# Performance work log

Hardware: AMD Instinct MI355X
Metric: run time of the kernel (lower is better)

## Reference

```python
import jax, jax.numpy as jnp
from jax import lax
import numpy as np

# ---- module hyperparameters (from init_kwargs) ----
DIM = 256
DIM_HEAD = 64
HEADS = 4
GROUPS = 4                      # offset_groups (defaults to heads)
INNER = DIM_HEAD * HEADS        # 256
OFF_DIMS = INNER // GROUPS      # 64
DOWN = 4
KS = 6
PAD = (KS - DOWN) // 2          # 1
OFFSET_SCALE = float(DOWN)      # offset_scale defaults to down_sample_factor
CPB_DIM = DIM // 4              # 64
SCALE = DIM_HEAD ** -0.5


def make_grid(h, w, dtype):
    # torch.meshgrid(arange(w), arange(h), indexing='xy') stacked at dim 0:
    # channel 0 = x (column index), channel 1 = y (row index); shape [2,h,w]
    yy, xx = jnp.meshgrid(jnp.arange(h), jnp.arange(w), indexing='ij')
    return jnp.stack([xx, yy], axis=0).astype(dtype)


def normalize_grid_c(vg):
    # vg: [..., 2, h, w] -> [..., h, w, 2]; faithful to source: channel 0
    # normalized by (h-1), channel 1 by (w-1) (source's h/w naming quirk).
    h, w = vg.shape[-2:]
    gh = 2.0 * vg[..., 0, :, :] / max(h - 1, 1) - 1.0
    gw = 2.0 * vg[..., 1, :, :] / max(w - 1, 1) - 1.0
    return jnp.stack([gh, gw], axis=-1)


def grid_sample_zeros(img, grid):
    # F.grid_sample bilinear, padding_mode='zeros', align_corners=False
    # img: [N,C,H,W]; grid: [N,Hg,Wg,2] with (..,0)=x, (..,1)=y in [-1,1]
    N, C, H, W = img.shape
    ix = ((grid[..., 0] + 1.0) * W - 1.0) * 0.5
    iy = ((grid[..., 1] + 1.0) * H - 1.0) * 0.5
    x0 = jnp.floor(ix)
    y0 = jnp.floor(iy)

    def gather(yy, xx):
        valid = (xx >= 0) & (xx <= W - 1) & (yy >= 0) & (yy <= H - 1)
        xc = jnp.clip(xx, 0, W - 1).astype(jnp.int32)
        yc = jnp.clip(yy, 0, H - 1).astype(jnp.int32)
        vals = jax.vmap(lambda im, y_, x_: im[:, y_, x_])(img, yc, xc)  # [N,C,Hg,Wg]
        return vals * valid[:, None, :, :].astype(img.dtype)

    wa = (x0 + 1 - ix) * (y0 + 1 - iy)
    wb = (ix - x0) * (y0 + 1 - iy)
    wc = (x0 + 1 - ix) * (iy - y0)
    wd = (ix - x0) * (iy - y0)
    return (gather(y0, x0) * wa[:, None]
            + gather(y0, x0 + 1) * wb[:, None]
            + gather(y0 + 1, x0) * wc[:, None]
            + gather(y0 + 1, x0 + 1) * wd[:, None])


def gconv1x1(t, w):
    # grouped 1x1 conv (no bias): t [b, G*Ci, h, w], w [G, Co, Ci]
    G, Co, Ci = w.shape
    bb, _, hh, ww = t.shape
    tg = t.reshape(bb, G, Ci, hh, ww)
    return jnp.einsum('bgihw,goi->bgohw', tg, w).reshape(bb, G * Co, hh, ww)


def setup_inputs() -> dict:
    key = jax.random.key(0)
    ks = jax.random.split(key, 12)
    s = 0.02
    B, H, W = 8, 32, 32
    cg = DIM // GROUPS  # per-group in-channels = 64
    og = INNER // GROUPS  # per-group out-channels = 64
    return {
        'x': jax.random.normal(ks[0], (B, DIM, H, W), jnp.float32),
        'wq': jax.random.normal(ks[1], (GROUPS, og, cg), jnp.float32) * s,
        'wk': jax.random.normal(ks[2], (GROUPS, og, cg), jnp.float32) * s,
        'wv': jax.random.normal(ks[3], (GROUPS, og, cg), jnp.float32) * s,
        'w_off_dw': jax.random.normal(ks[4], (OFF_DIMS, 1, KS, KS), jnp.float32) * s,
        'b_off_dw': jnp.zeros((OFF_DIMS,), jnp.float32),
        'w_off_pw': jax.random.normal(ks[5], (2, OFF_DIMS), jnp.float32) * s,
        'cpb_w1': jax.random.normal(ks[6], (CPB_DIM, 2), jnp.float32) * s,
        'cpb_b1': jnp.zeros((CPB_DIM,), jnp.float32),
        'cpb_w2': jax.random.normal(ks[7], (CPB_DIM, CPB_DIM), jnp.float32) * s,
        'cpb_b2': jnp.zeros((CPB_DIM,), jnp.float32),
        'cpb_w3': jax.random.normal(ks[8], (HEADS // GROUPS, CPB_DIM), jnp.float32) * s,
        'cpb_b3': jnp.zeros((HEADS // GROUPS,), jnp.float32),
        'w_out': jax.random.normal(ks[9], (DIM, INNER), jnp.float32) * s,
        'b_out': jnp.zeros((DIM,), jnp.float32),
    }


def reference(x, wq, wk, wv, w_off_dw, b_off_dw, w_off_pw,
              cpb_w1, cpb_b1, cpb_w2, cpb_b2, cpb_w3, cpb_b3,
              w_out, b_out):
    b, _, H, W = x.shape

    q = gconv1x1(x, wq)                                       # [b, INNER, H, W]
    gq = q.reshape(b * GROUPS, OFF_DIMS, H, W)                # grouped queries
    gx = x.reshape(b * GROUPS, DIM // GROUPS, H, W)           # grouped input

    # to_offsets: depthwise conv -> GELU -> 1x1 conv -> tanh -> scale
    off = lax.conv_general_dilated(
        gq, w_off_dw, window_strides=(DOWN, DOWN),
        padding=[(PAD, PAD), (PAD, PAD)],
        dimension_numbers=('NCHW', 'OIHW', 'NCHW'),
        feature_group_count=OFF_DIMS)
    off = off + b_off_dw[None, :, None, None]
    off = jax.nn.gelu(off, approximate=False)
    off = jnp.einsum('bchw,oc->bohw', off, w_off_pw)
    off = jnp.tanh(off) * OFFSET_SCALE                        # [bg, 2, h2, w2]

    h2, w2 = off.shape[-2:]
    vg = make_grid(h2, w2, off.dtype)[None] + off             # [bg, 2, h2, w2]
    vgs = normalize_grid_c(vg)                                # [bg, h2, w2, 2]

    kv = grid_sample_zeros(gx, vgs)                           # [bg, DIM/G, h2, w2]
    kv = kv.reshape(b, DIM, h2, w2)
    k = gconv1x1(kv, wk)
    v = gconv1x1(kv, wv)
    q = q * SCALE

    def to_heads(t):
        bb, _, hh, ww = t.shape
        return t.reshape(bb, HEADS, DIM_HEAD, hh * ww).transpose(0, 1, 3, 2)

    qh, kh, vh = to_heads(q), to_heads(k), to_heads(v)        # [b, h, i|j, d]
    sim = jnp.einsum('bhid,bhjd->bhij', qh, kh)               # [b, h, HW, h2*w2]

    # CPB relative position bias
    grid_q = normalize_grid_c(make_grid(H, W, x.dtype)).reshape(1, H * W, 2)
    grid_kv = vgs.reshape(b * GROUPS, h2 * w2, 2)
    pos = grid_q[:, :, None, :] - grid_kv[:, None, :, :]      # [bg, i, j, 2]
    bias = jnp.sign(pos) * jnp.log1p(jnp.abs(pos))
    bias = jax.nn.relu(bias @ cpb_w1.T + cpb_b1)
    bias = jax.nn.relu(bias @ cpb_w2.T + cpb_b2)
    bias = bias @ cpb_w3.T + cpb_b3                           # [bg, i, j, o]
    o = HEADS // GROUPS
    bias = bias.reshape(b, GROUPS, H * W, h2 * w2, o)
    bias = bias.transpose(0, 1, 4, 2, 3).reshape(b, HEADS, H * W, h2 * w2)

    attn = jax.nn.softmax(sim + bias, axis=-1)
    out = jnp.einsum('bhij,bhjd->bhid', attn, vh)             # [b, h, HW, d]
    out = out.transpose(0, 1, 3, 2).reshape(b, INNER, H, W)
    out = jnp.einsum('bchw,oc->bohw', out, w_out) + b_out[None, :, None, None]
    return out
```

## Files before the change

### kernel.cpp

```cpp
#include <hip/hip_runtime.h>
#include <hip/hip_bf16.h>
#include <math.h>

#define QSCALE 0.125f

typedef __attribute__((ext_vector_type(8))) short short8b;
typedef __attribute__((ext_vector_type(8))) _Float16 half8;
typedef __attribute__((ext_vector_type(2))) _Float16 half2v;
typedef __attribute__((ext_vector_type(4))) float f32x4;

__device__ __forceinline__ uint pack2(float a, float b) {
    uint r;
    asm("v_cvt_pk_bf16_f32 %0, %1, %2" : "=v"(r) : "v"(a), "v"(b));
    return r;
}
__device__ __forceinline__ uint pkrtz(float a, float b) {
    uint r;
    asm("v_cvt_pkrtz_f16_f32 %0, %1, %2" : "=v"(r) : "v"(a), "v"(b));
    return r;
}
__device__ __forceinline__ half2v h2(uint u) { return __builtin_bit_cast(half2v, u); }
__device__ __forceinline__ float slogf_(float p) {
    return copysignf(log1pf(fabsf(p)), p);
}

__global__ __launch_bounds__(256) void k_qproj(const float* __restrict__ x,
                                               const float* __restrict__ wq,
                                               float* __restrict__ q,
                                               short* __restrict__ qbt) {
    __shared__ float Wst[64 * 68];
    __shared__ float xs[64 * 68];
    int ht = blockIdx.x, g = blockIdx.y, b = blockIdx.z;
    int tid = threadIdx.x;
    for (int e = tid; e < 4096; e += 256) {
        int co = e >> 6, ci = e & 63;
        Wst[ci * 68 + co] = wq[(g * 64 + co) * 64 + ci];
    }
    const float* xb = x + (b * 256 + g * 64) * 1024 + ht * 64;
    for (int e = tid; e < 1024; e += 256) {
        int ci = e >> 4, hq = e & 15;
        *(float4*)&xs[ci * 68 + hq * 4] = *(const float4*)&xb[ci * 1024 + hq * 4];
    }
    __syncthreads();
    int cg = tid >> 4, hg = tid & 15;
    int co0 = cg * 4, hw0 = hg * 4;
    float acc[4][4] = {};
    for (int ci = 0; ci < 64; ci++) {
        float4 a4 = *(float4*)&Wst[ci * 68 + co0];
        float4 b4 = *(float4*)&xs[ci * 68 + hw0];
        float av[4] = {a4.x, a4.y, a4.z, a4.w};
        float bv[4] = {b4.x, b4.y, b4.z, b4.w};
        #pragma unroll
        for (int a = 0; a < 4; a++)
            #pragma unroll
            for (int c = 0; c < 4; c++) acc[a][c] += av[a] * bv[c];
    }
    float* qb = q + (b * 256 + g * 64) * 1024 + ht * 64;
    for (int a = 0; a < 4; a++) {
        float4 o = {acc[a][0], acc[a][1], acc[a][2], acc[a][3]};
        *(float4*)&qb[(co0 + a) * 1024 + hw0] = o;
    }
    short* q16 = qbt + ((size_t)((b * 4 + g) * 1024 + ht * 64)) * 64;
    for (int c = 0; c < 4; c++) {
        uint2 uu;
        uu.x = pack2(acc[0][c] * QSCALE, acc[1][c] * QSCALE);
        uu.y = pack2(acc[2][c] * QSCALE, acc[3][c] * QSCALE);
        *(uint2*)&q16[(hw0 + c) * 64 + co0] = uu;
    }
}

__global__ __launch_bounds__(256) void k_dw(const float* __restrict__ q,
                                            const float* __restrict__ wdw,
                                            const float* __restrict__ bdw,
                                            float* __restrict__ gdw) {
    __shared__ float qs[8 * 1024];
    __shared__ float wds[8 * 36];
    int cg = blockIdx.x, n = blockIdx.y;
    int b = n >> 2, gg = n & 3;
    int c0 = cg * 8;
    int tid = threadIdx.x;
    const float* qn = q + (b * 256 + gg * 64 + c0) * 1024;
    for (int e = tid; e < 2048; e += 256)
        ((float4*)qs)[e] = ((const float4*)qn)[e];
    for (int e = tid; e < 288; e += 256)
        wds[e] = wdw[c0 * 36 + e];
    __syncthreads();
    for (int e = tid; e < 512; e += 256) {
        int c = e >> 6, pos = e & 63;
        int oy = pos >> 3, ox = pos & 7;
        float acc = bdw[c0 + c];
        #pragma unroll
        for (int ky = 0; ky < 6; ky++) {
            int iy = oy * 4 - 1 + ky;
            if (iy < 0 || iy > 31) continue;
            #pragma unroll
            for (int kx = 0; kx < 6; kx++) {
                int ix = ox * 4 - 1 + kx;
                if (ix < 0 || ix > 31) continue;
                acc += qs[c * 1024 + iy * 32 + ix] * wds[c * 36 + ky * 6 + kx];
            }
        }
        gdw[(n * 64 + c0 + c) * 64 + pos] = acc * 0.5f * (1.f + erff(acc * 0.70710678118654752f));
    }
}

__global__ __launch_bounds__(256) void k_pre(const float* __restrict__ x,
                                             const float* __restrict__ gdw,
                                             const float* __restrict__ wpw,
                                             const float* __restrict__ wk,
                                             const float* __restrict__ wv,
                                             const float* __restrict__ wout,
                                             const float* __restrict__ w2,
                                             float* __restrict__ vgs,
                                             uint* __restrict__ u0g,
                                             short* __restrict__ kob,
                                             short* __restrict__ vob,
                                             short* __restrict__ wob,
                                             uint* __restrict__ w2h) {
    __shared__ float gstage[4096];
    __shared__ float kvsT[64 * 68];
    __shared__ uint wkh[64 * 36];
    __shared__ uint wvh[64 * 36];
    __shared__ uint kvh[64 * 36];
    __shared__ float vx_s[64], vy_s[64];
    int n = blockIdx.x, tid = threadIdx.x;
    int b = n >> 2, g = n & 3;

    {
        int e = n * 2048 + tid * 8;
        float4 f0 = *(const float4*)&wout[e];
        float4 f1 = *(const float4*)&wout[e + 4];
        uint4 u = {pack2(f0.x, f0.y), pack2(f0.z, f0.w), pack2(f1.x, f1.y), pack2(f1.z, f1.w)};
        *(uint4*)&wob[e] = u;
    }
    if (tid < 128) {
        int idx = n * 128 + tid;
        int c2 = idx >> 5, p = idx & 31;
        float2 wv2 = *(const float2*)&w2[c2 * 64 + 2 * p];
        w2h[c2 * 32 + p] = pkrtz(wv2.x, wv2.y);
    }
    for (int e = tid; e < 2048; e += 256) {
        int co = e >> 5, p = e & 31;
        float2 a = *(const float2*)&wk[(g * 64 + co) * 64 + 2 * p];
        float2 c = *(const float2*)&wv[(g * 64 + co) * 64 + 2 * p];
        wkh[co * 36 + p] = pkrtz(a.x, a.y);
        wvh[co * 36 + p] = pkrtz(c.x, c.y);
    }
    for (int e = tid; e < 1024; e += 256)
        ((float4*)gstage)[e] = ((const float4*)(gdw + n * 4096))[e];
    __syncthreads();
    if (tid < 128) {
        int o = tid >> 6, pos = tid & 63;
        float a = 0.f;
        #pragma unroll 8
        for (int c = 0; c < 64; c++) a += gstage[c * 64 + pos] * wpw[o * 64 + c];
        float off = tanhf(a) * 4.0f;
        if (o == 0) {
            int ox = pos & 7;
            float v = 2.f * ((float)ox + off) / 7.f - 1.f;
            vx_s[pos] = v;
            vgs[(n * 64 + pos) * 2] = v;
        } else {
            int oy = pos >> 3;
            float v = 2.f * ((float)oy + off) / 7.f - 1.f;
            vy_s[pos] = v;
            vgs[(n * 64 + pos) * 2 + 1] = v;
        }
    }
    __syncthreads();
    for (int e = tid; e < 2048; e += 256) {
        int ix = e >> 6, j = e & 63;
        float qx = (2.f / 31.f) * (float)ix - 1.f;
        float u = slogf_(qx - vx_s[j]);
        u0g[n * 2048 + e] = pkrtz(u, u);
    }
    for (int e = tid; e < 4096; e += 256) {
        int c = e >> 6, pos = e & 63;
        float ix = (vx_s[pos] + 1.f) * 16.f - 0.5f;
        float iy = (vy_s[pos] + 1.f) * 16.f - 0.5f;
        float x0 = floorf(ix), y0 = floorf(iy);
        float wa = (x0 + 1.f - ix) * (y0 + 1.f - iy);
        float wb = (ix - x0) * (y0 + 1.f - iy);
        float wc = (x0 + 1.f - ix) * (iy - y0);
        float wd = (ix - x0) * (iy - y0);
        const float* img = x + (b * 256 + g * 64 + c) * 1024;
        int xi = (int)x0, yi = (int)y0;
        float acc = 0.f;
        if (xi >= 0 && xi <= 31 && yi >= 0 && yi <= 31)             acc += img[yi * 32 + xi] * wa;
        if (xi + 1 >= 0 && xi + 1 <= 31 && yi >= 0 && yi <= 31)     acc += img[yi * 32 + xi + 1] * wb;
        if (xi >= 0 && xi <= 31 && yi + 1 >= 0 && yi + 1 <= 31)     acc += img[(yi + 1) * 32 + xi] * wc;
        if (xi + 1 >= 0 && xi + 1 <= 31 && yi + 1 >= 0 && yi + 1 <= 31) acc += img[(yi + 1) * 32 + xi + 1] * wd;
        kvsT[pos * 68 + c] = acc;
    }
    __syncthreads();
    for (int e = tid; e < 2048; e += 256) {
        int pos = e >> 5, p = e & 31;
        float2 v2 = *(const float2*)&kvsT[pos * 68 + 2 * p];
        kvh[pos * 36 + p] = pkrtz(v2.x, v2.y);
    }
    __syncthreads();
    int wid = tid >> 6, lane = tid & 63, lr = lane & 15, gq = lane >> 4;
    int mat = wid >> 1, cb = (wid & 1) * 32;
    const uint* wh = mat ? wvh : wkh;
    #pragma unroll
    for (int ct2 = 0; ct2 < 2; ct2++) {
        int ct = cb + ct2 * 16;
        half8 af[2];
        #pragma unroll
        for (int s = 0; s < 2; s++)
            af[s] = __builtin_bit_cast(half8, *(const uint4*)&wh[(ct + lr) * 36 + s * 16 + gq * 4]);
        #pragma unroll
        for (int nt = 0; nt < 4; nt++) {
            half8 bf[2];
            #pragma unroll
            for (int s = 0; s < 2; s++)
                bf[s] = __builtin_bit_cast(half8, *(const uint4*)&kvh[(nt * 16 + lr) * 36 + s * 16 + gq * 4]);
            f32x4 acc = {0.f, 0.f, 0.f, 0.f};
            acc = __builtin_amdgcn_mfma_f32_16x16x32_f16(af[0], bf[0], acc, 0, 0, 0);
            acc = __builtin_amdgcn_mfma_f32_16x16x32_f16(af[1], bf[1], acc, 0, 0, 0);
            if (mat == 0) {
                uint2 uu = {pack2(acc[0], acc[1]), pack2(acc[2], acc[3])};
                *(uint2*)&kob[n * 4096 + (nt * 16 + lr) * 64 + ct + gq * 4] = uu;
            } else {
                #pragma unroll
                for (int r = 0; r < 4; r++)
                    vob[n * 4096 + (ct + gq * 4 + r) * 64 + nt * 16 + lr] = (short)pack2(acc[r], acc[r]);
            }
        }
    }
}

__global__ __launch_bounds__(256) void k_cpb(const float* __restrict__ vgs,
                                             const uint* __restrict__ u0g,
                                             const float* __restrict__ w1,
                                             const float* __restrict__ b1,
                                             const uint* __restrict__ w2h,
                                             const float* __restrict__ b2,
                                             const float* __restrict__ w3,
                                             const float* __restrict__ b3,
                                             const short* __restrict__ qbt,
                                             const short* __restrict__ kob,
                                             const short* __restrict__ vob,
                                             short* __restrict__ attb) {
    __shared__ uint Q1p[64 * 36];
    __shared__ uint u0p[16 * 64];
    __shared__ float u1t[64];
    __shared__ uint w1ps[32];
    __shared__ float w3s[64];
    __shared__ float b2s[64];
    __shared__ float biasS[16 * 68];
    int iy = blockIdx.x >> 1, xh = blockIdx.x & 1, n = blockIdx.y, tid = threadIdx.x;
    float qy = 2.f * (float)iy / 31.f - 1.f;

    if (tid < 64) u1t[tid] = slogf_(qy - vgs[(n << 7) + tid * 2 + 1]);
    if (tid >= 64 && tid < 96) {
        int p = tid - 64;
        int s = p >> 4, gg = (p >> 2) & 3, pp = p & 3;
        int k = s * 32 + gg * 8 + 2 * pp;
        w1ps[p] = pkrtz(w1[2 * k], w1[2 * k + 2]);
    }
    if (tid >= 128 && tid < 192) w3s[tid - 128] = w3[tid - 128];
    if (tid >= 192) b2s[tid - 192] = b2[tid - 192];
    __syncthreads();
    for (int e = tid; e < 2048; e += 256) {
        int j = e >> 5, pp = e & 31;
        int k = pp * 2;
        float lo = fmaf(w1[2 * k + 1], u1t[j], b1[k]);
        float hi = fmaf(w1[2 * k + 3], u1t[j], b1[k + 1]);
        Q1p[j * 36 + pp] = pkrtz(lo, hi);
    }
    for (int e = tid; e < 1024; e += 256)
        u0p[e] = u0g[n * 2048 + xh * 1024 + e];

    int wid = tid >> 6, lane = tid & 63, lr = lane & 15, g = lane >> 4;
    float b3v = b3[0];

    half8 w2f[4][2];
    #pragma unroll
    for (int m = 0; m < 4; m++)
        #pragma unroll
        for (int s = 0; s < 2; s++)
            w2f[m][s] = __builtin_bit_cast(half8,
                *(const uint4*)&w2h[(m * 16 + lr) * 32 + s * 16 + g * 4]);
    __syncthreads();

    const half2v hz = {(_Float16)0, (_Float16)0};
    for (int ii = 0; ii < 4; ii++) {
        int ixl = wid * 4 + ii;
        #pragma unroll
        for (int nt = 0; nt < 4; nt++) {
            half2v u0v = h2(u0p[ixl * 64 + nt * 16 + lr]);
            const uint* q1p = &Q1p[(nt * 16 + lr) * 36];
            half8 bfr[2];
            #pragma unroll
            for (int s = 0; s < 2; s++) {
                uint4 q4 = *(const uint4*)&q1p[s * 16 + g * 4];
                uint4 wp4 = *(const uint4*)&w1ps[s * 16 + g * 4];
                half2v h0 = __builtin_elementwise_max(h2(wp4.x) * u0v + h2(q4.x), hz);
                half2v h1v = __builtin_elementwise_max(h2(wp4.y) * u0v + h2(q4.y), hz);
                half2v h2v_ = __builtin_elementwise_max(h2(wp4.z) * u0v + h2(q4.z), hz);
                half2v h3 = __builtin_elementwise_max(h2(wp4.w) * u0v + h2(q4.w), hz);
                uint4 hb = {__builtin_bit_cast(uint, h0), __builtin_bit_cast(uint, h1v),
                            __builtin_bit_cast(uint, h2v_), __builtin_bit_cast(uint, h3)};
                bfr[s] = __builtin_bit_cast(half8, hb);
            }
            f32x4 acc[4];
            #pragma unroll
            for (int m = 0; m < 4; m++) {
                f32x4 cseed = *(const f32x4*)&b2s[m * 16 + g * 4];
                acc[m] = __builtin_amdgcn_mfma_f32_16x16x32_f16(w2f[m][0], bfr[0], cseed, 0, 0, 0);
            }
            #pragma unroll
            for (int m = 0; m < 4; m++)
                acc[m] = __builtin_amdgcn_mfma_f32_16x16x32_f16(w2f[m][1], bfr[1], acc[m], 0, 0, 0);
            f32x4 tv = {0.f, 0.f, 0.f, 0.f};
            #pragma unroll
            for (int m = 0; m < 4; m++) {
                f32x4 r = __builtin_elementwise_max(acc[m], (f32x4){0.f, 0.f, 0.f, 0.f});
                f32x4 w3m = *(const f32x4*)&w3s[m * 16 + g * 4];
                tv += w3m * r;
            }
            float t = (tv[0] + tv[1]) + (tv[2] + tv[3]);
            t += __shfl_xor(t, 16);
            t += __shfl_xor(t, 32);
            if (g == nt) biasS[ixl * 68 + lane] = t + b3v;
        }
    }
    __syncthreads();

    if (wid == 0) {
        float* P = biasS;
        int i0w = iy * 32 + xh * 16;
        const short* kb = kob + n * 4096;
        const short* vb = vob + n * 4096;
        const short* qb = qbt + ((size_t)n * 1024 + i0w + lr) * 64;
        short8b qf[2];
        qf[0] = *(const short8b*)&qb[g * 8];
        qf[1] = *(const short8b*)&qb[32 + g * 8];
        float bv[4][4];
        #pragma unroll
        for (int r = 0; r < 4; r++)
            #pragma unroll
            for (int nt = 0; nt < 4; nt++)
                bv[r][nt] = biasS[(g * 4 + r) * 68 + nt * 16 + lr];

        f32x4 acc[4];
        #pragma unroll
        for (int nt = 0; nt < 4; nt++) {
            short8b kf0 = *(const short8b*)&kb[(nt * 16 + lr) * 64 + g * 8];
            short8b kf1 = *(const short8b*)&kb[(nt * 16 + lr) * 64 + 32 + g * 8];
            acc[nt] = (f32x4){0.f, 0.f, 0.f, 0.f};
            acc[nt] = __builtin_amdgcn_mfma_f32_16x16x32_bf16(qf[0], kf0, acc[nt], 0, 0, 0);
            acc[nt] = __builtin_amdgcn_mfma_f32_16x16x32_bf16(qf[1], kf1, acc[nt], 0, 0, 0);
        }
        #pragma unroll
        for (int r = 0; r < 4; r++) {
            float s0 = acc[0][r] + bv[r][0], s1 = acc[1][r] + bv[r][1];
            float s2 = acc[2][r] + bv[r][2], s3 = acc[3][r] + bv[r][3];
            float m = fmaxf(fmaxf(s0, s1), fmaxf(s2, s3));
            m = fmaxf(m, __shfl_xor(m, 1));
            m = fmaxf(m, __shfl_xor(m, 2));
            m = fmaxf(m, __shfl_xor(m, 4));
            m = fmaxf(m, __shfl_xor(m, 8));
            float e0 = __expf(s0 - m), e1 = __expf(s1 - m);
            float e2 = __expf(s2 - m), e3 = __expf(s3 - m);
            float sum = (e0 + e1) + (e2 + e3);
            sum += __shfl_xor(sum, 1);
            sum += __shfl_xor(sum, 2);
            sum += __shfl_xor(sum, 4);
            sum += __shfl_xor(sum, 8);
            float inv = 1.f / sum;
            int row = g * 4 + r;
            P[row * 68 + lr]      = e0 * inv;
            P[row * 68 + 16 + lr] = e1 * inv;
            P[row * 68 + 32 + lr] = e2 * inv;
            P[row * 68 + 48 + lr] = e3 * inv;
        }
        const float* pr = &P[lr * 68];
        float4 a0 = *(float4*)&pr[g * 8];
        float4 a1 = *(float4*)&pr[g * 8 + 4];
        float4 a2 = *(float4*)&pr[32 + g * 8];
        float4 a3 = *(float4*)&pr[32 + g * 8 + 4];
        uint4 up0 = {pack2(a0.x, a0.y), pack2(a0.z, a0.w), pack2(a1.x, a1.y), pack2(a1.z, a1.w)};
        uint4 up1 = {pack2(a2.x, a2.y), pack2(a2.z, a2.w), pack2(a3.x, a3.y), pack2(a3.z, a3.w)};
        short8b pf0 = __builtin_bit_cast(short8b, up0);
        short8b pf1 = __builtin_bit_cast(short8b, up1);

        f32x4 oacc[4];
        #pragma unroll
        for (int nt = 0; nt < 4; nt++) {
            short8b vf0 = *(const short8b*)&vb[(nt * 16 + lr) * 64 + g * 8];
            short8b vf1 = *(const short8b*)&vb[(nt * 16 + lr) * 64 + 32 + g * 8];
            oacc[nt] = (f32x4){0.f, 0.f, 0.f, 0.f};
            oacc[nt] = __builtin_amdgcn_mfma_f32_16x16x32_bf16(pf0, vf0, oacc[nt], 0, 0, 0);
            oacc[nt] = __builtin_amdgcn_mfma_f32_16x16x32_bf16(pf1, vf1, oacc[nt], 0, 0, 0);
        }
        #pragma unroll
        for (int nt = 0; nt < 4; nt++)
            #pragma unroll
            for (int r = 0; r < 4; r++)
                P[(nt * 16 + lr) * 17 + g * 4 + r] = oacc[nt][r];
        int il = lane >> 2, dq = lane & 3;
        uint ub[8];
        #pragma unroll
        for (int t = 0; t < 8; t++) {
            float lo = P[(dq * 16 + 2 * t) * 17 + il];
            float hi = P[(dq * 16 + 2 * t + 1) * 17 + il];
            ub[t] = pack2(lo, hi);
        }
        int b_ = n >> 2, h_ = n & 3;
        short* op = attb + ((size_t)(b_ * 1024 + i0w + il)) * 256 + h_ * 64 + dq * 16;
        uint4 s0v = {ub[0], ub[1], ub[2], ub[3]};
        uint4 s1v = {ub[4], ub[5], ub[6], ub[7]};
        ((uint4*)op)[0] = s0v;
        ((uint4*)op)[1] = s1v;
    }
}

__global__ __launch_bounds__(256) void k_outproj(const short* __restrict__ attb,
                                                 const short* __restrict__ wob,
                                                 const float* __restrict__ bout,
                                                 float* __restrict__ y) {
    int rt = blockIdx.x;
    int ct = blockIdx.y;
    int tid = threadIdx.x, wid = tid >> 6, lane = tid & 63, lr = lane & 15, g = lane >> 4;
    int wr = wid >> 1, wc = wid & 1;
    int b = rt >> 5;
    int hw0 = (rt & 31) * 32 + wr * 16;
    int cobase = ct * 128 + wc * 64;
    const short* arow = attb + ((size_t)(b * 1024) + hw0) * 256;
    const short* brow = wob + (size_t)cobase * 256;

    f32x4 acc[4];
    #pragma unroll
    for (int nn = 0; nn < 4; nn++) acc[nn] = (f32x4){0.f, 0.f, 0.f, 0.f};
    #pragma unroll
    for (int s = 0; s < 8; s++) {
        short8b af = *(const short8b*)&arow[lr * 256 + s * 32 + g * 8];
        #pragma unroll
        for (int nn = 0; nn < 4; nn++) {
            short8b bf = *(const short8b*)&brow[(nn * 16 + lr) * 256 + s * 32 + g * 8];
            acc[nn] = __builtin_amdgcn_mfma_f32_16x16x32_bf16(af, bf, acc[nn], 0, 0, 0);
        }
    }
    #pragma unroll
    for (int nn = 0; nn < 4; nn++) {
        int co = cobase + nn * 16 + lr;
        float bo = bout[co];
        float4 o = {acc[nn][0] + bo, acc[nn][1] + bo, acc[nn][2] + bo, acc[nn][3] + bo};
        *(float4*)&y[(size_t)b * 262144 + (size_t)co * 1024 + hw0 + g * 4] = o;
    }
}

extern "C" void kernel_launch(void* const* d_in, const int* in_sizes, int n_in,
                              void* d_out, int out_size, void* d_ws, size_t ws_size,
                              hipStream_t stream) {
    const float* x    = (const float*)d_in[0];
    const float* wq   = (const float*)d_in[1];
    const float* wk   = (const float*)d_in[2];
    const float* wv   = (const float*)d_in[3];
    const float* wdw  = (const float*)d_in[4];
    const float* bdw  = (const float*)d_in[5];
    const float* wpw  = (const float*)d_in[6];
    const float* cw1  = (const float*)d_in[7];
    const float* cb1  = (const float*)d_in[8];
    const float* cw2  = (const float*)d_in[9];
    const float* cb2  = (const float*)d_in[10];
    const float* cw3  = (const float*)d_in[11];
    const float* cb3  = (const float*)d_in[12];
    const float* wout = (const float*)d_in[13];
    const float* bout = (const float*)d_in[14];
    float* y  = (float*)d_out;
    float* ws = (float*)d_ws;

    float* q    = ws;
    short* attb = (short*)ws;
    float* vgs  = ws + 4325376;
    short* qbt  = (short*)(ws + 4329472);
    short* kob  = (short*)(ws + 5378048);
    short* vob  = (short*)(ws + 5443584);
    float* gdw  = ws + 5509120;
    short* wob  = (short*)(ws + 5640192);
    uint*  u0g  = (uint*)(ws + 5672960);
    uint*  w2h  = (uint*)(ws + 5738496);

    k_qproj  <<<dim3(16, 4, 8), 256, 0, stream>>>(x, wq, q, qbt);
    k_dw     <<<dim3(8, 32),    256, 0, stream>>>(q, wdw, bdw, gdw);
    k_pre    <<<32,             256, 0, stream>>>(x, gdw, wpw, wk, wv, wout, cw2,
                                                  vgs, u0g, kob, vob, wob, w2h);
    k_cpb    <<<dim3(64, 32),   256, 0, stream>>>(vgs, u0g, cw1, cb1, w2h, cb2, cw3, cb3,
                                                  qbt, kob, vob, attb);
    k_outproj<<<dim3(256, 2),   256, 0, stream>>>(attb, wob, bout, y);
}
```

Baseline: 100.4 us.

## Process full query row per k_cpb block and stage W2 in LDS

Each k_cpb block now covers a full query row of 32 positions instead of half a row, which halves the grid. The shared setup work (u1/Q1 tables, loading weights) is amortized over twice as many positions. W2 fragments are now staged in padded shared memory and reloaded per MFMA instead of being held in registers, likely to cut register pressure. Two waves now run the attention tail instead of one. This trades fewer blocks, and so less parallelism, plus extra LDS reads for less redundant setup.

Result: faster. 97.07 us (-3.3%).

```diff
diff --git a/kernel.cpp b/kernel.cpp
--- a/kernel.cpp
+++ b/kernel.cpp
@@ -243,13 +243,14 @@
                                              const short* __restrict__ vob,
                                              short* __restrict__ attb) {
     __shared__ uint Q1p[64 * 36];
-    __shared__ uint u0p[16 * 64];
+    __shared__ uint u0p[32 * 64];
+    __shared__ uint w2s[64 * 36];
     __shared__ float u1t[64];
     __shared__ uint w1ps[32];
     __shared__ float w3s[64];
     __shared__ float b2s[64];
-    __shared__ float biasS[16 * 68];
-    int iy = blockIdx.x >> 1, xh = blockIdx.x & 1, n = blockIdx.y, tid = threadIdx.x;
+    __shared__ float biasS[32 * 68];
+    int iy = blockIdx.x, n = blockIdx.y, tid = threadIdx.x;
     float qy = 2.f * (float)iy / 31.f - 1.f;
 
     if (tid < 64) u1t[tid] = slogf_(qy - vgs[(n << 7) + tid * 2 + 1]);
@@ -269,24 +270,18 @@
         float hi = fmaf(w1[2 * k + 3], u1t[j], b1[k + 1]);
         Q1p[j * 36 + pp] = pkrtz(lo, hi);
     }
-    for (int e = tid; e < 1024; e += 256)
-        u0p[e] = u0g[n * 2048 + xh * 1024 + e];
+    for (int e = tid; e < 2048; e += 256)
+        w2s[(e >> 5) * 36 + (e & 31)] = w2h[e];
+    for (int e = tid; e < 2048; e += 256)
+        u0p[e] = u0g[n * 2048 + e];
 
     int wid = tid >> 6, lane = tid & 63, lr = lane & 15, g = lane >> 4;
     float b3v = b3[0];
-
-    half8 w2f[4][2];
-    #pragma unroll
-    for (int m = 0; m < 4; m++)
-        #pragma unroll
-        for (int s = 0; s < 2; s++)
-            w2f[m][s] = __builtin_bit_cast(half8,
-                *(const uint4*)&w2h[(m * 16 + lr) * 32 + s * 16 + g * 4]);
     __syncthreads();
 
     const half2v hz = {(_Float16)0, (_Float16)0};
-    for (int ii = 0; ii < 4; ii++) {
-        int ixl = wid * 4 + ii;
+    for (int ii = 0; ii < 8; ii++) {
+        int ixl = wid * 8 + ii;
         #pragma unroll
         for (int nt = 0; nt < 4; nt++) {
             half2v u0v = h2(u0p[ixl * 64 + nt * 16 + lr]);
@@ -307,12 +302,17 @@
             f32x4 acc[4];
             #pragma unroll
             for (int m = 0; m < 4; m++) {
+                half8 w2f0 = __builtin_bit_cast(half8,
+                    *(const uint4*)&w2s[(m * 16 + lr) * 36 + g * 4]);
                 f32x4 cseed = *(const f32x4*)&b2s[m * 16 + g * 4];
-                acc[m] = __builtin_amdgcn_mfma_f32_16x16x32_f16(w2f[m][0], bfr[0], cseed, 0, 0, 0);
-            }
-            #pragma unroll
-            for (int m = 0; m < 4; m++)
-                acc[m] = __builtin_amdgcn_mfma_f32_16x16x32_f16(w2f[m][1], bfr[1], acc[m], 0, 0, 0);
+                acc[m] = __builtin_amdgcn_mfma_f32_16x16x32_f16(w2f0, bfr[0], cseed, 0, 0, 0);
+            }
+            #pragma unroll
+            for (int m = 0; m < 4; m++) {
+                half8 w2f1 = __builtin_bit_cast(half8,
+                    *(const uint4*)&w2s[(m * 16 + lr) * 36 + 16 + g * 4]);
+                acc[m] = __builtin_amdgcn_mfma_f32_16x16x32_f16(w2f1, bfr[1], acc[m], 0, 0, 0);
+            }
             f32x4 tv = {0.f, 0.f, 0.f, 0.f};
             #pragma unroll
             for (int m = 0; m < 4; m++) {
@@ -328,9 +328,10 @@
     }
     __syncthreads();
 
-    if (wid == 0) {
-        float* P = biasS;
-        int i0w = iy * 32 + xh * 16;
+    if (wid < 2) {
+        int lb = wid * 16;
+        float* P = &biasS[lb * 68];
+        int i0w = iy * 32 + lb;
         const short* kb = kob + n * 4096;
         const short* vb = vob + n * 4096;
         const short* qb = qbt + ((size_t)n * 1024 + i0w + lr) * 64;
@@ -342,7 +343,7 @@
         for (int r = 0; r < 4; r++)
             #pragma unroll
             for (int nt = 0; nt < 4; nt++)
-                bv[r][nt] = biasS[(g * 4 + r) * 68 + nt * 16 + lr];
+                bv[r][nt] = biasS[(lb + g * 4 + r) * 68 + nt * 16 + lr];
 
         f32x4 acc[4];
         #pragma unroll
@@ -488,7 +489,7 @@
     k_dw     <<<dim3(8, 32),    256, 0, stream>>>(q, wdw, bdw, gdw);
     k_pre    <<<32,             256, 0, stream>>>(x, gdw, wpw, wk, wv, wout, cw2,
                                                   vgs, u0g, kob, vob, wob, w2h);
-    k_cpb    <<<dim3(64, 32),   256, 0, stream>>>(vgs, u0g, cw1, cb1, w2h, cb2, cw3, cb3,
+    k_cpb    <<<dim3(32, 32),   256, 0, stream>>>(vgs, u0g, cw1, cb1, w2h, cb2, cw3, cb3,
                                                   qbt, kob, vob, attb);
     k_outproj<<<dim3(256, 2),   256, 0, stream>>>(attb, wob, bout, y);
 }
```
